# Kernel tuning notes

Measured on AMD Instinct MI355X. Metric: run time of the kernel, lower is better.

The kernel has to match this reference:

```python
import jax, jax.numpy as jnp
import numpy as np

B, T, C = 16, 4096, 128
CODEBOOK_SIZE = 1024


def setup_inputs() -> dict:
    key = jax.random.key(0)
    kx, ke = jax.random.split(key)
    x = jax.random.normal(kx, (B, T, C), dtype=jnp.float32)
    embed = jax.random.normal(ke, (CODEBOOK_SIZE, C), dtype=jnp.float32)
    return {"x": x, "embed": embed}


def reference(x, embed):
    # x: [B, T, C], embed: [K, C]
    b, t, c = x.shape
    flat = x.reshape(b * t, c)                      # [BT, C]
    # distance = -||x - e||^2, expanded so we never materialize [BT, K, C]
    x_sq = jnp.sum(flat * flat, axis=-1, keepdims=True)   # [BT, 1]
    e_sq = jnp.sum(embed * embed, axis=-1)                 # [K]
    dist = 2.0 * (flat @ embed.T) - x_sq - e_sq[None, :]   # [BT, K]
    embed_ind = jnp.argmax(dist, axis=-1).reshape(b, t)    # [B, T]
    quantized = embed[embed_ind]                           # [B, T, C] gather
    return quantized, embed_ind
```

## Files before the change

### kernel.cpp

```cpp
#include <hip/hip_runtime.h>
#include <float.h>


#define Cdim        128
#define KCODES      1024
#define CH          64
#define NCH         16
#define BROWS       128
#define THREADS     256
#define IMG_OFF     4096
#define CHUNK_BYTES 32768

typedef _Float16 f16;
typedef __attribute__((ext_vector_type(8)))  _Float16 f16x8;
typedef __attribute__((ext_vector_type(16))) float    f32x16;

__global__ __launch_bounds__(256) void esq_kernel(const float* __restrict__ embed,
                                                  float* __restrict__ esq, int K) {
    int gid  = blockIdx.x * blockDim.x + threadIdx.x;
    int code = gid >> 6;
    int lane = threadIdx.x & 63;
    if (code >= K) return;
    float2 v = ((const float2*)(embed + (size_t)code * Cdim))[lane];
    float  s = fmaf(v.x, v.x, v.y * v.y);
    #pragma unroll
    for (int m = 32; m >= 1; m >>= 1) s += __shfl_xor(s, m, 64);
    if (lane == 0) esq[code] = s;
}

__device__ __forceinline__ void cvt8s(float4 a, float4 b, float scale,
                                      f16x8& h, f16x8& lo) {
    float v[8] = {a.x, a.y, a.z, a.w, b.x, b.y, b.z, b.w};
    #pragma unroll
    for (int i = 0; i < 8; ++i) {
        float s = v[i] * scale;
        f16 hh = (f16)s;
        h[i]  = hh;
        lo[i] = (f16)(s - (float)hh);
    }
}

__global__ __launch_bounds__(256) void bconv_kernel(const float* __restrict__ embed,
                                                    char* __restrict__ ws) {
    int t    = blockIdx.x * 256 + threadIdx.x;
    int code = t >> 4;
    int slot = t & 15;
    int kk   = slot >> 1;
    int lh   = slot & 1;
    int ch = code >> 6, nt = (code >> 5) & 1, lm = code & 31;
    const float4* p = (const float4*)(embed + (size_t)code * Cdim + kk * 16 + lh * 8);
    f16x8 h, lo;
    cvt8s(p[0], p[1], 1.0f, h, lo);
    size_t base = (size_t)IMG_OFF + (size_t)ch * CHUNK_BYTES + nt * 16384
                + kk * 1024 + lh * 512 + lm * 16;
    *(f16x8*)(ws + base)        = h;
    *(f16x8*)(ws + base + 8192) = lo;
}

__device__ __forceinline__ void gll16(const void* g, void* l) {
    __builtin_amdgcn_global_load_lds(
        (const __attribute__((address_space(1))) unsigned int*)g,
        (__attribute__((address_space(3))) unsigned int*)l, 16, 0, 0);
}

__global__ __launch_bounds__(THREADS, 2) void vq_kernel(
    const float* __restrict__ x, const float* __restrict__ embed,
    const char* __restrict__ ws, float* __restrict__ outq,
    float* __restrict__ outi) {

    __shared__ __align__(16) char  Bb[2][CHUNK_BYTES];
    __shared__ __align__(16) float esq_lds[KCODES];
    __shared__ float mrg_v[2][BROWS];
    __shared__ int   mrg_i[2][BROWS];
    __shared__ int   winners[BROWS];

    const int tid  = threadIdx.x;
    const int wid  = tid >> 6;
    const int l    = tid & 63;
    const int lm   = l & 31;
    const int lh   = l >> 5;
    const int wr   = wid & 1;
    const int nt   = wid >> 1;
    const int row0 = blockIdx.x * BROWS;
    const int loff = lh * 512 + lm * 16;

    {
        const char* src = ws + IMG_OFF + wid * 8192 + (size_t)l * 16;
        char*       dst = &Bb[0][wid * 8192];
        #pragma unroll
        for (int i = 0; i < 8; ++i) gll16(src + i * 1024, dst + i * 1024);
        gll16(ws + wid * 1024 + (size_t)l * 16, (char*)esq_lds + wid * 1024);
    }

    f16x8 bxh[2][8], bxl[2][8];
    #pragma unroll
    for (int n = 0; n < 2; ++n) {
        const float* xr = x + (size_t)(row0 + wr * 64 + n * 32 + lm) * Cdim + lh * 8;
        #pragma unroll
        for (int kk = 0; kk < 8; ++kk) {
            float4 v0 = *(const float4*)(xr + kk * 16);
            float4 v1 = *(const float4*)(xr + kk * 16 + 4);
            cvt8s(v0, v1, 2.0f, bxh[n][kk], bxl[n][kk]);
        }
    }

    float best0 = -FLT_MAX, best1 = -FLT_MAX;
    int   bidx0 = 0,        bidx1 = 0;

    auto compute = [&](int ch, f32x16& A0, f32x16& A1) {
        const int cur = ch & 1, nxt = cur ^ 1;
        __builtin_amdgcn_s_barrier();
        if (ch + 1 < NCH) {
            const char* src = ws + IMG_OFF + (size_t)(ch + 1) * CHUNK_BYTES
                            + wid * 8192 + (size_t)l * 16;
            char* dst = &Bb[nxt][wid * 8192];
            #pragma unroll
            for (int i = 0; i < 8; ++i) gll16(src + i * 1024, dst + i * 1024);
            asm volatile("s_waitcnt vmcnt(8)" ::: "memory");
        } else {
            asm volatile("s_waitcnt vmcnt(0)" ::: "memory");
        }
        __builtin_amdgcn_s_barrier();

        #pragma unroll
        for (int r = 0; r < 16; ++r) { A0[r] = 0.f; A1[r] = 0.f; }

        const char* bbA = &Bb[cur][nt * 16384 + loff];
        f16x8 aeh = *(const f16x8*)(bbA);
        f16x8 ael = *(const f16x8*)(bbA + 8192);
        __builtin_amdgcn_s_setprio(1);
        #pragma unroll
        for (int kk = 0; kk < 8; ++kk) {
            f16x8 aehN, aelN;
            if (kk < 7) {
                aehN = *(const f16x8*)(bbA + (kk + 1) * 1024);
                aelN = *(const f16x8*)(bbA + 8192 + (kk + 1) * 1024);
            }
            A0 = __builtin_amdgcn_mfma_f32_32x32x16_f16(aeh, bxh[0][kk], A0, 0, 0, 0);
            A1 = __builtin_amdgcn_mfma_f32_32x32x16_f16(aeh, bxh[1][kk], A1, 0, 0, 0);
            A0 = __builtin_amdgcn_mfma_f32_32x32x16_f16(ael, bxh[0][kk], A0, 0, 0, 0);
            A1 = __builtin_amdgcn_mfma_f32_32x32x16_f16(ael, bxh[1][kk], A1, 0, 0, 0);
            A0 = __builtin_amdgcn_mfma_f32_32x32x16_f16(aeh, bxl[0][kk], A0, 0, 0, 0);
            A1 = __builtin_amdgcn_mfma_f32_32x32x16_f16(aeh, bxl[1][kk], A1, 0, 0, 0);
            aeh = aehN; ael = aelN;
        }
        __builtin_amdgcn_s_setprio(0);
    };

    auto score = [&](int ch, const f32x16& A0, const f32x16& A1) {
        const int cb = ch * CH + nt * 32 + lh * 4;
        #pragma unroll
        for (int g = 0; g < 4; ++g) {
            float4 e4 = *(const float4*)&esq_lds[cb + g * 8];
            #pragma unroll
            for (int j = 0; j < 4; ++j) {
                const int r = g * 4 + j;
                const int code = cb + g * 8 + j;
                float s0 = A0[r] - ((const float*)&e4)[j];
                float s1 = A1[r] - ((const float*)&e4)[j];
                if (s0 > best0) { best0 = s0; bidx0 = code; }
                if (s1 > best1) { best1 = s1; bidx1 = code; }
            }
        }
    };

    f32x16 aA0, aA1, aB0, aB1;
    compute(0, aA0, aA1);
    #pragma unroll 1
    for (int b = 0; b < 7; ++b) {
        compute(2 * b + 1, aB0, aB1);
        score  (2 * b,     aA0, aA1);
        compute(2 * b + 2, aA0, aA1);
        score  (2 * b + 1, aB0, aB1);
    }
    compute(15, aB0, aB1);
    score  (14, aA0, aA1);
    score  (15, aB0, aB1);

    {
        float v; int vi;
        v = __shfl_xor(best0, 32, 64); vi = __shfl_xor(bidx0, 32, 64);
        if (v > best0 || (v == best0 && vi < bidx0)) { best0 = v; bidx0 = vi; }
        v = __shfl_xor(best1, 32, 64); vi = __shfl_xor(bidx1, 32, 64);
        if (v > best1 || (v == best1 && vi < bidx1)) { best1 = v; bidx1 = vi; }
    }
    if (lh == 0) {
        mrg_v[nt][wr * 64 + lm]      = best0;  mrg_i[nt][wr * 64 + lm]      = bidx0;
        mrg_v[nt][wr * 64 + 32 + lm] = best1;  mrg_i[nt][wr * 64 + 32 + lm] = bidx1;
    }
    __syncthreads();
    if (tid < BROWS) {
        float v0 = mrg_v[0][tid]; int i0 = mrg_i[0][tid];
        float v1 = mrg_v[1][tid]; int i1 = mrg_i[1][tid];
        int bi = (v1 > v0 || (v1 == v0 && i1 < i0)) ? i1 : i0;
        winners[tid] = bi;
        outi[row0 + tid] = (float)bi;
    }
    __syncthreads();

    #pragma unroll
    for (int i = 0; i < 16; ++i) {
        int pos = i * THREADS + tid;
        int r = pos >> 5, c4 = pos & 31;
        int idx = winners[r];
        float4 v = ((const float4*)(embed + (size_t)idx * Cdim))[c4];
        ((float4*)(outq + (size_t)(row0 + r) * Cdim))[c4] = v;
    }
}

extern "C" void kernel_launch(void* const* d_in, const int* in_sizes, int n_in,
                              void* d_out, int out_size, void* d_ws, size_t ws_size,
                              hipStream_t stream) {
    const float* x     = (const float*)d_in[0];
    const float* embed = (const float*)d_in[1];
    const int M = in_sizes[0] / Cdim;
    const int K = in_sizes[1] / Cdim;
    float* outq = (float*)d_out;
    float* outi = outq + (size_t)M * Cdim;

    esq_kernel <<<K / 4, 256, 0, stream>>>(embed, (float*)d_ws, K);
    bconv_kernel<<<64, 256, 0, stream>>>(embed, (char*)d_ws);
    vq_kernel  <<<M / BROWS, THREADS, 0, stream>>>(x, embed, (const char*)d_ws,
                                                   outq, outi);
}
```

Measured before the change: 68.90 us.

## Switch VQ distance GEMM to 16x16x32 MFMA with matching codebook layout

Replaces the 32x32x16 f16 MFMA tiles with 16x16x32 MFMA tiles. Each wave now computes 2 code tiles by 4 row tiles, and the precomputed codebook image in the workspace is relaid out to match. The compute/score software pipeline across chunks is dropped in favour of a simple loop, and the final argmax reduction uses two lane shuffles. The intent is a cheaper MFMA shape with less accumulator pressure and fewer dependent MFMA chains. In exchange, scoring no longer overlaps with the next chunk's MFMA work.

```diff
diff --git a/kernel.cpp b/kernel.cpp
--- a/kernel.cpp
+++ b/kernel.cpp
@@ -12,8 +12,10 @@
 #define CHUNK_BYTES 32768
 
 typedef _Float16 f16;
-typedef __attribute__((ext_vector_type(8)))  _Float16 f16x8;
-typedef __attribute__((ext_vector_type(16))) float    f32x16;
+typedef __attribute__((ext_vector_type(8))) _Float16 f16x8;
+typedef __attribute__((ext_vector_type(4))) float    f32x4;
+
+#define MFMA16(A, B, C) __builtin_amdgcn_mfma_f32_16x16x32_f16((A), (B), (C), 0, 0, 0)
 
 __global__ __launch_bounds__(256) void esq_kernel(const float* __restrict__ embed,
                                                   float* __restrict__ esq, int K) {
@@ -44,17 +46,17 @@
                                                     char* __restrict__ ws) {
     int t    = blockIdx.x * 256 + threadIdx.x;
     int code = t >> 4;
-    int slot = t & 15;
-    int kk   = slot >> 1;
-    int lh   = slot & 1;
-    int ch = code >> 6, nt = (code >> 5) & 1, lm = code & 31;
-    const float4* p = (const float4*)(embed + (size_t)code * Cdim + kk * 16 + lh * 8);
+    int seg  = t & 15;
+    int ks   = seg >> 2;
+    int kseg = seg & 3;
+    int ch = code >> 6, ctg = (code >> 4) & 3, lr = code & 15;
+    const float4* p = (const float4*)(embed + (size_t)code * Cdim + ks * 32 + kseg * 8);
     f16x8 h, lo;
     cvt8s(p[0], p[1], 1.0f, h, lo);
-    size_t base = (size_t)IMG_OFF + (size_t)ch * CHUNK_BYTES + nt * 16384
-                + kk * 1024 + lh * 512 + lm * 16;
-    *(f16x8*)(ws + base)        = h;
-    *(f16x8*)(ws + base + 8192) = lo;
+    size_t base = (size_t)IMG_OFF + (size_t)ch * CHUNK_BYTES
+                + (ctg * 4 + ks) * 1024 + (kseg * 16 + lr) * 16;
+    *(f16x8*)(ws + base)         = h;
+    *(f16x8*)(ws + base + 16384) = lo;
 }
 
 __device__ __forceinline__ void gll16(const void* g, void* l) {
@@ -77,12 +79,11 @@
     const int tid  = threadIdx.x;
     const int wid  = tid >> 6;
     const int l    = tid & 63;
-    const int lm   = l & 31;
-    const int lh   = l >> 5;
+    const int lr   = l & 15;
+    const int lg   = l >> 4;
     const int wr   = wid & 1;
     const int nt   = wid >> 1;
     const int row0 = blockIdx.x * BROWS;
-    const int loff = lh * 512 + lm * 16;
 
     {
         const char* src = ws + IMG_OFF + wid * 8192 + (size_t)l * 16;
@@ -92,23 +93,27 @@
         gll16(ws + wid * 1024 + (size_t)l * 16, (char*)esq_lds + wid * 1024);
     }
 
-    f16x8 bxh[2][8], bxl[2][8];
-    #pragma unroll
-    for (int n = 0; n < 2; ++n) {
-        const float* xr = x + (size_t)(row0 + wr * 64 + n * 32 + lm) * Cdim + lh * 8;
-        #pragma unroll
-        for (int kk = 0; kk < 8; ++kk) {
-            float4 v0 = *(const float4*)(xr + kk * 16);
-            float4 v1 = *(const float4*)(xr + kk * 16 + 4);
-            cvt8s(v0, v1, 2.0f, bxh[n][kk], bxl[n][kk]);
-        }
-    }
-
-    float best0 = -FLT_MAX, best1 = -FLT_MAX;
-    int   bidx0 = 0,        bidx1 = 0;
-
-    auto compute = [&](int ch, f32x16& A0, f32x16& A1) {
+    f16x8 bxh[4][4], bxl[4][4];
+    #pragma unroll
+    for (int rt = 0; rt < 4; ++rt) {
+        const float* xr = x + (size_t)(row0 + wr * 64 + rt * 16 + lr) * Cdim + lg * 8;
+        #pragma unroll
+        for (int ks = 0; ks < 4; ++ks) {
+            float4 v0 = *(const float4*)(xr + ks * 32);
+            float4 v1 = *(const float4*)(xr + ks * 32 + 4);
+            cvt8s(v0, v1, 2.0f, bxh[rt][ks], bxl[rt][ks]);
+        }
+    }
+
+    float best[4];
+    int   bidx[4];
+    #pragma unroll
+    for (int rt = 0; rt < 4; ++rt) { best[rt] = -FLT_MAX; bidx[rt] = 0; }
+
+    #pragma unroll 1
+    for (int ch = 0; ch < NCH; ++ch) {
         const int cur = ch & 1, nxt = cur ^ 1;
+
         __builtin_amdgcn_s_barrier();
         if (ch + 1 < NCH) {
             const char* src = ws + IMG_OFF + (size_t)(ch + 1) * CHUNK_BYTES
@@ -122,71 +127,66 @@
         }
         __builtin_amdgcn_s_barrier();
 
-        #pragma unroll
-        for (int r = 0; r < 16; ++r) { A0[r] = 0.f; A1[r] = 0.f; }
-
-        const char* bbA = &Bb[cur][nt * 16384 + loff];
-        f16x8 aeh = *(const f16x8*)(bbA);
-        f16x8 ael = *(const f16x8*)(bbA + 8192);
-        __builtin_amdgcn_s_setprio(1);
-        #pragma unroll
-        for (int kk = 0; kk < 8; ++kk) {
-            f16x8 aehN, aelN;
-            if (kk < 7) {
-                aehN = *(const f16x8*)(bbA + (kk + 1) * 1024);
-                aelN = *(const f16x8*)(bbA + 8192 + (kk + 1) * 1024);
+        f32x4 acc[2][4];
+        #pragma unroll
+        for (int ct = 0; ct < 2; ++ct)
+            #pragma unroll
+            for (int rt = 0; rt < 4; ++rt)
+                acc[ct][rt] = (f32x4){0.f, 0.f, 0.f, 0.f};
+
+        const char* bb = &Bb[cur][(size_t)l * 16];
+
+        #pragma unroll
+        for (int ks = 0; ks < 4; ++ks) {
+            f16x8 eh0 = *(const f16x8*)(bb + ((nt * 2 + 0) * 4 + ks) * 1024);
+            f16x8 el0 = *(const f16x8*)(bb + ((nt * 2 + 0) * 4 + ks) * 1024 + 16384);
+            f16x8 eh1 = *(const f16x8*)(bb + ((nt * 2 + 1) * 4 + ks) * 1024);
+            f16x8 el1 = *(const f16x8*)(bb + ((nt * 2 + 1) * 4 + ks) * 1024 + 16384);
+
+            __builtin_amdgcn_s_setprio(1);
+            #pragma unroll
+            for (int rt = 0; rt < 4; ++rt) acc[0][rt] = MFMA16(eh0, bxh[rt][ks], acc[0][rt]);
+            #pragma unroll
+            for (int rt = 0; rt < 4; ++rt) acc[1][rt] = MFMA16(eh1, bxh[rt][ks], acc[1][rt]);
+            #pragma unroll
+            for (int rt = 0; rt < 4; ++rt) acc[0][rt] = MFMA16(eh0, bxl[rt][ks], acc[0][rt]);
+            #pragma unroll
+            for (int rt = 0; rt < 4; ++rt) acc[1][rt] = MFMA16(eh1, bxl[rt][ks], acc[1][rt]);
+            #pragma unroll
+            for (int rt = 0; rt < 4; ++rt) acc[0][rt] = MFMA16(el0, bxh[rt][ks], acc[0][rt]);
+            #pragma unroll
+            for (int rt = 0; rt < 4; ++rt) acc[1][rt] = MFMA16(el1, bxh[rt][ks], acc[1][rt]);
+            __builtin_amdgcn_s_setprio(0);
+        }
+
+        #pragma unroll
+        for (int ct = 0; ct < 2; ++ct) {
+            const int cb = ch * CH + (nt * 2 + ct) * 16 + lg * 4;
+            float4 e4 = *(const float4*)&esq_lds[cb];
+            #pragma unroll
+            for (int rt = 0; rt < 4; ++rt) {
+                #pragma unroll
+                for (int j = 0; j < 4; ++j) {
+                    float s = acc[ct][rt][j] - ((const float*)&e4)[j];
+                    if (s > best[rt]) { best[rt] = s; bidx[rt] = cb + j; }
+                }
             }
-            A0 = __builtin_amdgcn_mfma_f32_32x32x16_f16(aeh, bxh[0][kk], A0, 0, 0, 0);
-            A1 = __builtin_amdgcn_mfma_f32_32x32x16_f16(aeh, bxh[1][kk], A1, 0, 0, 0);
-            A0 = __builtin_amdgcn_mfma_f32_32x32x16_f16(ael, bxh[0][kk], A0, 0, 0, 0);
-            A1 = __builtin_amdgcn_mfma_f32_32x32x16_f16(ael, bxh[1][kk], A1, 0, 0, 0);
-            A0 = __builtin_amdgcn_mfma_f32_32x32x16_f16(aeh, bxl[0][kk], A0, 0, 0, 0);
-            A1 = __builtin_amdgcn_mfma_f32_32x32x16_f16(aeh, bxl[1][kk], A1, 0, 0, 0);
-            aeh = aehN; ael = aelN;
-        }
-        __builtin_amdgcn_s_setprio(0);
-    };
-
-    auto score = [&](int ch, const f32x16& A0, const f32x16& A1) {
-        const int cb = ch * CH + nt * 32 + lh * 4;
-        #pragma unroll
-        for (int g = 0; g < 4; ++g) {
-            float4 e4 = *(const float4*)&esq_lds[cb + g * 8];
-            #pragma unroll
-            for (int j = 0; j < 4; ++j) {
-                const int r = g * 4 + j;
-                const int code = cb + g * 8 + j;
-                float s0 = A0[r] - ((const float*)&e4)[j];
-                float s1 = A1[r] - ((const float*)&e4)[j];
-                if (s0 > best0) { best0 = s0; bidx0 = code; }
-                if (s1 > best1) { best1 = s1; bidx1 = code; }
-            }
-        }
-    };
-
-    f32x16 aA0, aA1, aB0, aB1;
-    compute(0, aA0, aA1);
-    #pragma unroll 1
-    for (int b = 0; b < 7; ++b) {
-        compute(2 * b + 1, aB0, aB1);
-        score  (2 * b,     aA0, aA1);
-        compute(2 * b + 2, aA0, aA1);
-        score  (2 * b + 1, aB0, aB1);
-    }
-    compute(15, aB0, aB1);
-    score  (14, aA0, aA1);
-    score  (15, aB0, aB1);
-
-    {
-        float v; int vi;
-        v = __shfl_xor(best0, 32, 64); vi = __shfl_xor(bidx0, 32, 64);
-        if (v > best0 || (v == best0 && vi < bidx0)) { best0 = v; bidx0 = vi; }
-        v = __shfl_xor(best1, 32, 64); vi = __shfl_xor(bidx1, 32, 64);
-        if (v > best1 || (v == best1 && vi < bidx1)) { best1 = v; bidx1 = vi; }
-    }
-    if (lh == 0) {
-        mrg_v[nt][wr * 64 + lm]      = best0;  mrg_i[nt][wr * 64 + lm]      = bidx0;
-        mrg_v[nt][wr * 64 + 32 + lm] = best1;  mrg_i[nt][wr * 64 + 32 + lm] = bidx1;
+        }
+    }
+
+    #pragma unroll
+    for (int rt = 0; rt < 4; ++rt) {
+        float bs = best[rt]; int bi = bidx[rt];
+        #pragma unroll
+        for (int m = 16; m <= 32; m <<= 1) {
+            float vs = __shfl_xor(bs, m, 64);
+            int   vi = __shfl_xor(bi, m, 64);
+            if (vs > bs || (vs == bs && vi < bi)) { bs = vs; bi = vi; }
+        }
+        if (lg == 0) {
+            mrg_v[nt][wr * 64 + rt * 16 + lr] = bs;
+            mrg_i[nt][wr * 64 + rt * 16 + lr] = bi;
+        }
     }
     __syncthreads();
     if (tid < BROWS) {
```

New measurement: 61.44 us. 10.8% less time.
